# Kernel optimization log

Measured on AMD Instinct MI355X. Metric: run time of the kernel, lower is better.

The kernel has to match this reference:

```python
import jax, jax.numpy as jnp
import numpy as np

EPS = 1e-12  # torch F.normalize eps

def _l2norm(v, axis):
    n = jnp.sqrt(jnp.sum(v * v, axis=axis, keepdims=True))
    return v / jnp.maximum(n, EPS)

def setup_inputs() -> dict:
    key = jax.random.key(0)
    k1, k2, k3 = jax.random.split(key, 3)
    N, C, H, W, K = 64, 512, 32, 32, 64
    x = jax.random.normal(k1, (N, C, H, W), dtype=jnp.float32)
    conv_w = jax.random.normal(k2, (K, C), dtype=jnp.float32) * 0.05
    centroids = jax.random.uniform(k3, (K, C), dtype=jnp.float32)
    return {"x": x, "conv_w": conv_w, "centroids": centroids}

def reference(x, conv_w, centroids):
    N, C, H, W = x.shape
    K = centroids.shape[0]
    # descriptor-wise L2 normalization over channel dim
    x = _l2norm(x, axis=1)
    xf = x.reshape(N, C, H * W)                       # (N, C, S)
    # 1x1 conv (no bias) == per-pixel matmul, then softmax over clusters
    logits = jnp.einsum('kc,ncs->nks', conv_w, xf)    # (N, K, S)
    a = jax.nn.softmax(logits, axis=1)                # softmax over clusters
    # vlad[n,k,:] = sum_s a[n,k,s] * (x[n,:,s] - centroid[k])
    # = (a @ x^T) - centroid * sum_s a   -- two GEMM-like ops, no (N,K,C,S) tensor
    vlad = jnp.einsum('nks,ncs->nkc', a, xf) - a.sum(axis=-1)[..., None] * centroids[None, :, :]
    # intra-normalization per cluster, flatten, global L2 norm
    vlad = _l2norm(vlad, axis=2)
    vlad = vlad.reshape(N, K * C)
    vlad = _l2norm(vlad, axis=1)
    return vlad
```

## Files before the change

### kernel.cpp

```cpp
#include <hip/hip_runtime.h>
#include <hip/hip_bf16.h>
#include <math.h>

#define EPSF 1e-12f

typedef __attribute__((ext_vector_type(8))) short bf16x8;
typedef __attribute__((ext_vector_type(4))) float f32x4;
typedef __attribute__((ext_vector_type(4))) short short4v;
typedef __attribute__((ext_vector_type(4))) unsigned short ushort4v;

static __device__ __forceinline__ short f2bf(float f) {
  union { __hip_bfloat16 h; short s; } u;
  u.h = __float2bfloat16(f);
  return u.s;
}

__global__ __launch_bounds__(256) void k2_mfma(
    const float* __restrict__ x, const float* __restrict__ w,
    unsigned short* __restrict__ ap, float* __restrict__ suma) {
  __shared__ __align__(16) float xf[64][70];
  __shared__ __align__(16) short wb[64][72];
  __shared__ __align__(16) float red[4][64];
  __shared__ float invs[64];
  __shared__ float gmaxs[64];
  __shared__ float gsums[64];

  const int n = blockIdx.y;
  const int s0 = blockIdx.x << 6;
  const int t = threadIdx.x;
  const int lane = t & 63;
  const int wid = t >> 6;
  const int col = t & 15;
  const int quad = (t >> 4) & 3;
  const int cr = t >> 4;
  const int sg = t & 15;

  f32x4 acc[4] = {{0,0,0,0},{0,0,0,0},{0,0,0,0},{0,0,0,0}};
  float ssq0 = 0.f, ssq1 = 0.f, ssq2 = 0.f, ssq3 = 0.f;

  for (int c0 = 0; c0 < 512; c0 += 64) {
#pragma unroll
    for (int p = 0; p < 4; ++p) {
      int c = cr + (p << 4);
      float4 g = *(const float4*)&x[((size_t)((n << 9) + c0 + c) << 10) + s0 + (sg << 2)];
      float2 glo; glo.x = g.x; glo.y = g.y;
      float2 ghi; ghi.x = g.z; ghi.y = g.w;
      *(float2*)&xf[c][sg << 2] = glo;
      *(float2*)&xf[c][(sg << 2) + 2] = ghi;
      ssq0 = fmaf(g.x, g.x, ssq0); ssq1 = fmaf(g.y, g.y, ssq1);
      ssq2 = fmaf(g.z, g.z, ssq2); ssq3 = fmaf(g.w, g.w, ssq3);
      float4 gw = *(const float4*)&w[(c << 9) + c0 + (sg << 2)];
      short4v hw; hw.x = f2bf(gw.x); hw.y = f2bf(gw.y); hw.z = f2bf(gw.z); hw.w = f2bf(gw.w);
      *(short4v*)&wb[c][sg << 2] = hw;
    }
    __syncthreads();
#pragma unroll
    for (int cc = 0; cc < 64; cc += 32) {
      bf16x8 af = *(const bf16x8*)&wb[(wid << 4) + col][cc + (quad << 3)];
      int cb = cc + (quad << 3);
#pragma unroll
      for (int sgr = 0; sgr < 4; ++sgr) {
        int sc = (sgr << 4) + col;
        bf16x8 bfr;
#pragma unroll
        for (int j = 0; j < 8; ++j) bfr[j] = f2bf(xf[cb + j][sc]);
        acc[sgr] = __builtin_amdgcn_mfma_f32_16x16x32_bf16(af, bfr, acc[sgr], 0, 0, 0);
      }
    }
    __syncthreads();
  }

  ssq0 += __shfl_xor(ssq0, 16, 64); ssq0 += __shfl_xor(ssq0, 32, 64);
  ssq1 += __shfl_xor(ssq1, 16, 64); ssq1 += __shfl_xor(ssq1, 32, 64);
  ssq2 += __shfl_xor(ssq2, 16, 64); ssq2 += __shfl_xor(ssq2, 32, 64);
  ssq3 += __shfl_xor(ssq3, 16, 64); ssq3 += __shfl_xor(ssq3, 32, 64);
  if (lane < 16) {
    float4 v; v.x = ssq0; v.y = ssq1; v.z = ssq2; v.w = ssq3;
    *(float4*)&red[wid][sg << 2] = v;
  }
  __syncthreads();
  if (t < 64) {
    float tot = red[0][t] + red[1][t] + red[2][t] + red[3][t];
    invs[t] = 1.0f / fmaxf(sqrtf(tot), EPSF);
  }
  __syncthreads();

  float li[4];
#pragma unroll
  for (int sgr = 0; sgr < 4; ++sgr) li[sgr] = invs[(sgr << 4) + col];
  float le[4][4];
#pragma unroll
  for (int sgr = 0; sgr < 4; ++sgr)
#pragma unroll
    for (int r = 0; r < 4; ++r) le[sgr][r] = acc[sgr][r] * li[sgr];

  float mx[4];
#pragma unroll
  for (int sgr = 0; sgr < 4; ++sgr) {
    float m = fmaxf(fmaxf(le[sgr][0], le[sgr][1]), fmaxf(le[sgr][2], le[sgr][3]));
    m = fmaxf(m, __shfl_xor(m, 16, 64));
    m = fmaxf(m, __shfl_xor(m, 32, 64));
    mx[sgr] = m;
  }
  if (lane < 16) {
#pragma unroll
    for (int sgr = 0; sgr < 4; ++sgr) red[wid][(sgr << 4) + sg] = mx[sgr];
  }
  __syncthreads();
  if (t < 64)
    gmaxs[t] = fmaxf(fmaxf(red[0][t], red[1][t]), fmaxf(red[2][t], red[3][t]));
  __syncthreads();

  float ps[4];
#pragma unroll
  for (int sgr = 0; sgr < 4; ++sgr) {
    float gm = gmaxs[(sgr << 4) + col];
    float p = 0.f;
#pragma unroll
    for (int r = 0; r < 4; ++r) {
      float e = __expf(le[sgr][r] - gm);
      le[sgr][r] = e;
      p += e;
    }
    p += __shfl_xor(p, 16, 64);
    p += __shfl_xor(p, 32, 64);
    ps[sgr] = p;
  }
  if (lane < 16) {
#pragma unroll
    for (int sgr = 0; sgr < 4; ++sgr) red[wid][(sgr << 4) + sg] = ps[sgr];
  }
  __syncthreads();
  if (t < 64) gsums[t] = red[0][t] + red[1][t] + red[2][t] + red[3][t];
  __syncthreads();

  float sk[4] = {0.f, 0.f, 0.f, 0.f};
#pragma unroll
  for (int sgr = 0; sgr < 4; ++sgr) {
    float rinv = 1.0f / gsums[(sgr << 4) + col];
#pragma unroll
    for (int r = 0; r < 4; ++r) {
      float av = le[sgr][r] * rinv;
      sk[r] += av;
      float apv = av * li[sgr];
      int k = (wid << 4) + (quad << 2) + r;
      ap[((size_t)((n << 6) + k) << 10) + s0 + (sgr << 4) + col] =
          (unsigned short)f2bf(apv);
    }
  }
#pragma unroll
  for (int r = 0; r < 4; ++r) {
    sk[r] += __shfl_xor(sk[r], 1, 64);
    sk[r] += __shfl_xor(sk[r], 2, 64);
    sk[r] += __shfl_xor(sk[r], 4, 64);
    sk[r] += __shfl_xor(sk[r], 8, 64);
  }
  if (col == 0) {
#pragma unroll
    for (int r = 0; r < 4; ++r)
      atomicAdd(&suma[(n << 6) + (wid << 4) + (quad << 2) + r], sk[r]);
  }
}

#define K3_LOADT(gx, ga, S0)                                                   \
  do {                                                                         \
    _Pragma("unroll") for (int p = 0; p < 4; ++p) {                            \
      gx[p] = *(const float4*)(xbase + ((size_t)(p << 4) << 10) + (S0));       \
      ga[p] = *(const ushort4v*)(abase + ((size_t)(p << 4) << 10) + (S0));     \
    }                                                                          \
  } while (0)

#define K3_WRITET(gx, ga)                                                      \
  do {                                                                         \
    _Pragma("unroll") for (int p = 0; p < 4; ++p) {                            \
      int c = cr + (p << 4);                                                   \
      short4v hx;                                                              \
      hx.x = f2bf(gx[p].x); hx.y = f2bf(gx[p].y);                              \
      hx.z = f2bf(gx[p].z); hx.w = f2bf(gx[p].w);                              \
      *(short4v*)&xb[c][sg << 2] = hx;                                         \
      *(ushort4v*)&at[c][sg << 2] = ga[p];                                     \
    }                                                                          \
  } while (0)

#define K3_MFMAT()                                                             \
  do {                                                                         \
    _Pragma("unroll") for (int ss = 0; ss < 64; ss += 32) {                    \
      bf16x8 af = *(const bf16x8*)&xb[(wid << 4) + col][ss + (quad << 3)];     \
      _Pragma("unroll") for (int kt = 0; kt < 4; ++kt) {                       \
        bf16x8 bfr = *(const bf16x8*)&at[(kt << 4) + col][ss + (quad << 3)];   \
        acc[kt] = __builtin_amdgcn_mfma_f32_16x16x32_bf16(af, bfr, acc[kt], 0, 0, 0); \
      }                                                                        \
    }                                                                          \
  } while (0)

__global__ __launch_bounds__(256) void k3_mfma(
    const float* __restrict__ x, const unsigned short* __restrict__ ap,
    const float* __restrict__ cent, const float* __restrict__ suma,
    float* __restrict__ out, float* __restrict__ rnorm2) {
  __shared__ __align__(16) char sm[64 * 72 * 2 * 2];
  short (*xb)[72] = reinterpret_cast<short(*)[72]>(sm);
  short (*at)[72] = reinterpret_cast<short(*)[72]>(sm + 9216);
  float (*lt)[68] = reinterpret_cast<float(*)[68]>(sm);

  const int n = blockIdx.x;
  const int c0 = blockIdx.y << 6;
  const int t = threadIdx.x;
  const int lane = t & 63;
  const int wid = t >> 6;
  const int col = t & 15;
  const int quad = (t >> 4) & 3;
  const int cr = t >> 4;
  const int sg = t & 15;

  f32x4 acc[4] = {{0,0,0,0},{0,0,0,0},{0,0,0,0},{0,0,0,0}};

  const float* xbase = &x[((size_t)((n << 9) + c0 + cr) << 10) + (sg << 2)];
  const unsigned short* abase = &ap[((size_t)((n << 6) + cr) << 10) + (sg << 2)];

  float4 gxA[4]; ushort4v gaA[4];
  float4 gxB[4]; ushort4v gaB[4];

  K3_LOADT(gxA, gaA, 0);
#pragma unroll 1
  for (int it = 0; it < 8; ++it) {
    K3_WRITET(gxA, gaA);
    __syncthreads();
    K3_LOADT(gxB, gaB, (size_t)(((it << 1) + 1) << 6));
    K3_MFMAT();
    __syncthreads();
    K3_WRITET(gxB, gaB);
    __syncthreads();
    if (it < 7) {
      K3_LOADT(gxA, gaA, (size_t)(((it << 1) + 2) << 6));
    }
    K3_MFMAT();
    __syncthreads();
  }

  float sa[4];
#pragma unroll
  for (int kt = 0; kt < 4; ++kt) sa[kt] = suma[(n << 6) + (kt << 4) + col];
  const int crow = (wid << 4) + (quad << 2);
  float r2[4] = {0.f, 0.f, 0.f, 0.f};
#pragma unroll
  for (int kt = 0; kt < 4; ++kt) {
    int k = (kt << 4) + col;
#pragma unroll
    for (int r = 0; r < 4; ++r) {
      int c = crow + r;
      float ce = cent[(k << 9) + c0 + c];
      float val = acc[kt][r] - sa[kt] * ce;
      r2[kt] = fmaf(val, val, r2[kt]);
      lt[k][c] = val;
    }
  }
#pragma unroll
  for (int kt = 0; kt < 4; ++kt) {
    r2[kt] += __shfl_xor(r2[kt], 16, 64);
    r2[kt] += __shfl_xor(r2[kt], 32, 64);
  }
  if (lane < 16) {
#pragma unroll
    for (int kt = 0; kt < 4; ++kt)
      atomicAdd(&rnorm2[(n << 6) + (kt << 4) + sg], r2[kt]);
  }
  __syncthreads();
#pragma unroll
  for (int u = 0; u < 4; ++u) {
    int k = t >> 2;
    int c = ((t & 3) << 2) + (u << 4);
    float4 v = *(const float4*)&lt[k][c];
    *(float4*)&out[((size_t)((n << 6) + k) << 9) + c0 + c] = v;
  }
}

__global__ __launch_bounds__(256) void k5_scale(const float* __restrict__ vlad,
                                                const float* __restrict__ rnorm2,
                                                float* __restrict__ out) {
  __shared__ float gsh;
  const int b = blockIdx.x;
  const int t = threadIdx.x;
  const int n = b >> 5;
  if (t < 64) {
    float rn = sqrtf(rnorm2[(n << 6) + t]);
    float nr = rn / fmaxf(rn, EPSF);
    float g = nr * nr;
#pragma unroll
    for (int off = 32; off > 0; off >>= 1) g += __shfl_xor(g, off, 64);
    if (t == 0) gsh = g;
  }
  __syncthreads();
  const float ginv = 1.0f / fmaxf(sqrtf(gsh), EPSF);
  const int idx = (b << 8) + t;
  const int kg = idx >> 7;
  float rn = sqrtf(rnorm2[kg]);
  float f = (1.0f / fmaxf(rn, EPSF)) * ginv;
  float4 v = ((const float4*)vlad)[idx];
  float4 o;
  o.x = v.x * f; o.y = v.y * f; o.z = v.z * f; o.w = v.w * f;
  ((float4*)out)[idx] = o;
}

extern "C" void kernel_launch(void* const* d_in, const int* in_sizes, int n_in,
                              void* d_out, int out_size, void* d_ws, size_t ws_size,
                              hipStream_t stream) {
  (void)in_sizes; (void)n_in; (void)out_size; (void)ws_size;
  const float* x = (const float*)d_in[0];
  const float* w = (const float*)d_in[1];
  const float* cent = (const float*)d_in[2];
  float* out = (float*)d_out;

  float* ws = (float*)d_ws;
  float* suma = ws;
  float* rnorm2 = ws + 4096;
  unsigned short* ap = (unsigned short*)(ws + 12288);

  hipMemsetAsync(ws, 0, 8192 * sizeof(float), stream);
  k2_mfma<<<dim3(16, 64), 256, 0, stream>>>(x, w, ap, suma);
  k3_mfma<<<dim3(64, 8), 256, 0, stream>>>(x, ap, cent, suma, out, rnorm2);
  k5_scale<<<2048, 256, 0, stream>>>(out, rnorm2, out);
}
```

Before: 229.4 us.

## Halve k3 channel tile to 32, double grid, double-buffer LDS tiles

The second GEMM kernel now covers 32 channels per block instead of 64, which doubles the grid to 1024 blocks for better CU occupancy. Each wave now computes a 16x32 output sub-tile, and the 64-wide spatial tiles are double-buffered in shared memory, removing one barrier per stage. Launch bounds request four blocks per CU. The cost is that each assignment tile is re-read twice as often, and the per-block epilogue is smaller.

```diff
diff --git a/kernel.cpp b/kernel.cpp
--- a/kernel.cpp
+++ b/kernel.cpp
@@ -162,115 +162,118 @@
   }
 }
 
-#define K3_LOADT(gx, ga, S0)                                                   \
+#define K3_LOADT(GX0, GX1, GA0, GA1, TI)                                       \
   do {                                                                         \
-    _Pragma("unroll") for (int p = 0; p < 4; ++p) {                            \
-      gx[p] = *(const float4*)(xbase + ((size_t)(p << 4) << 10) + (S0));       \
-      ga[p] = *(const ushort4v*)(abase + ((size_t)(p << 4) << 10) + (S0));     \
-    }                                                                          \
+    const int so_ = (TI) << 6;                                                 \
+    GX0 = *(const float4*)(xbase + so_);                                       \
+    GX1 = *(const float4*)(xbase + so_ + 32);                                  \
+    GA0 = *(const bf16x8*)(abase + so_);                                       \
+    GA1 = *(const bf16x8*)(abase + so_ + 32);                                  \
   } while (0)
 
-#define K3_WRITET(gx, ga)                                                      \
+#define K3_WRITET(GX0, GX1, GA0, GA1, XB, AT)                                  \
   do {                                                                         \
-    _Pragma("unroll") for (int p = 0; p < 4; ++p) {                            \
-      int c = cr + (p << 4);                                                   \
-      short4v hx;                                                              \
-      hx.x = f2bf(gx[p].x); hx.y = f2bf(gx[p].y);                              \
-      hx.z = f2bf(gx[p].z); hx.w = f2bf(gx[p].w);                              \
-      *(short4v*)&xb[c][sg << 2] = hx;                                         \
-      *(ushort4v*)&at[c][sg << 2] = ga[p];                                     \
-    }                                                                          \
+    short4v h0, h1;                                                            \
+    h0.x = f2bf(GX0.x); h0.y = f2bf(GX0.y); h0.z = f2bf(GX0.z); h0.w = f2bf(GX0.w); \
+    h1.x = f2bf(GX1.x); h1.y = f2bf(GX1.y); h1.z = f2bf(GX1.z); h1.w = f2bf(GX1.w); \
+    *(short4v*)&XB[t >> 3][(t & 7) << 2] = h0;                                 \
+    *(short4v*)&XB[t >> 3][((t & 7) << 2) + 32] = h1;                          \
+    *(bf16x8*)&AT[t >> 2][(t & 3) << 3] = GA0;                                 \
+    *(bf16x8*)&AT[t >> 2][((t & 3) << 3) + 32] = GA1;                          \
   } while (0)
 
-#define K3_MFMAT()                                                             \
+#define K3_MFMAT(XB, AT)                                                       \
   do {                                                                         \
     _Pragma("unroll") for (int ss = 0; ss < 64; ss += 32) {                    \
-      bf16x8 af = *(const bf16x8*)&xb[(wid << 4) + col][ss + (quad << 3)];     \
-      _Pragma("unroll") for (int kt = 0; kt < 4; ++kt) {                       \
-        bf16x8 bfr = *(const bf16x8*)&at[(kt << 4) + col][ss + (quad << 3)];   \
+      bf16x8 af = *(const bf16x8*)&XB[cb + col][ss + (quad << 3)];             \
+      _Pragma("unroll") for (int kt = 0; kt < 2; ++kt) {                       \
+        bf16x8 bfr = *(const bf16x8*)&AT[kb + (kt << 4) + col][ss + (quad << 3)]; \
         acc[kt] = __builtin_amdgcn_mfma_f32_16x16x32_bf16(af, bfr, acc[kt], 0, 0, 0); \
       }                                                                        \
     }                                                                          \
   } while (0)
 
-__global__ __launch_bounds__(256) void k3_mfma(
+__global__ __launch_bounds__(256, 4) void k3_mfma(
     const float* __restrict__ x, const unsigned short* __restrict__ ap,
     const float* __restrict__ cent, const float* __restrict__ suma,
     float* __restrict__ out, float* __restrict__ rnorm2) {
-  __shared__ __align__(16) char sm[64 * 72 * 2 * 2];
-  short (*xb)[72] = reinterpret_cast<short(*)[72]>(sm);
-  short (*at)[72] = reinterpret_cast<short(*)[72]>(sm + 9216);
-  float (*lt)[68] = reinterpret_cast<float(*)[68]>(sm);
+  __shared__ __align__(16) char sm[27648];
+  short (*xb0)[72] = reinterpret_cast<short(*)[72]>(sm);
+  short (*at0)[72] = reinterpret_cast<short(*)[72]>(sm + 4608);
+  short (*xb1)[72] = reinterpret_cast<short(*)[72]>(sm + 13824);
+  short (*at1)[72] = reinterpret_cast<short(*)[72]>(sm + 18432);
+  float (*lt)[36] = reinterpret_cast<float(*)[36]>(sm);
 
   const int n = blockIdx.x;
-  const int c0 = blockIdx.y << 6;
+  const int c0 = blockIdx.y << 5;
   const int t = threadIdx.x;
   const int lane = t & 63;
   const int wid = t >> 6;
   const int col = t & 15;
   const int quad = (t >> 4) & 3;
-  const int cr = t >> 4;
   const int sg = t & 15;
-
-  f32x4 acc[4] = {{0,0,0,0},{0,0,0,0},{0,0,0,0},{0,0,0,0}};
-
-  const float* xbase = &x[((size_t)((n << 9) + c0 + cr) << 10) + (sg << 2)];
-  const unsigned short* abase = &ap[((size_t)((n << 6) + cr) << 10) + (sg << 2)];
-
-  float4 gxA[4]; ushort4v gaA[4];
-  float4 gxB[4]; ushort4v gaB[4];
-
-  K3_LOADT(gxA, gaA, 0);
+  const int cb = (wid & 1) << 4;
+  const int kb = (wid >> 1) << 5;
+
+  f32x4 acc[2] = {{0, 0, 0, 0}, {0, 0, 0, 0}};
+
+  const float* xbase = &x[((size_t)((n << 9) + c0 + (t >> 3)) << 10) + ((t & 7) << 2)];
+  const unsigned short* abase = &ap[((size_t)((n << 6) + (t >> 2)) << 10) + ((t & 3) << 3)];
+
+  float4 xA0, xA1, xB0, xB1;
+  bf16x8 aA0, aA1, aB0, aB1;
+
+  K3_LOADT(xA0, xA1, aA0, aA1, 0);
+  K3_WRITET(xA0, xA1, aA0, aA1, xb0, at0);
+  K3_LOADT(xB0, xB1, aB0, aB1, 1);
+  __syncthreads();
+
 #pragma unroll 1
-  for (int it = 0; it < 8; ++it) {
-    K3_WRITET(gxA, gaA);
+  for (int it = 0; it < 16; it += 2) {
+    const bool last = (it == 14);
+    K3_WRITET(xB0, xB1, aB0, aB1, xb1, at1);
+    if (!last) K3_LOADT(xA0, xA1, aA0, aA1, it + 2);
+    K3_MFMAT(xb0, at0);
     __syncthreads();
-    K3_LOADT(gxB, gaB, (size_t)(((it << 1) + 1) << 6));
-    K3_MFMAT();
+    if (!last) {
+      K3_WRITET(xA0, xA1, aA0, aA1, xb0, at0);
+      K3_LOADT(xB0, xB1, aB0, aB1, it + 3);
+    }
+    K3_MFMAT(xb1, at1);
     __syncthreads();
-    K3_WRITET(gxB, gaB);
-    __syncthreads();
-    if (it < 7) {
-      K3_LOADT(gxA, gaA, (size_t)(((it << 1) + 2) << 6));
-    }
-    K3_MFMAT();
-    __syncthreads();
-  }
-
-  float sa[4];
-#pragma unroll
-  for (int kt = 0; kt < 4; ++kt) sa[kt] = suma[(n << 6) + (kt << 4) + col];
-  const int crow = (wid << 4) + (quad << 2);
-  float r2[4] = {0.f, 0.f, 0.f, 0.f};
-#pragma unroll
-  for (int kt = 0; kt < 4; ++kt) {
-    int k = (kt << 4) + col;
-#pragma unroll
-    for (int r = 0; r < 4; ++r) {
-      int c = crow + r;
-      float ce = cent[(k << 9) + c0 + c];
-      float val = acc[kt][r] - sa[kt] * ce;
-      r2[kt] = fmaf(val, val, r2[kt]);
-      lt[k][c] = val;
-    }
-  }
-#pragma unroll
-  for (int kt = 0; kt < 4; ++kt) {
-    r2[kt] += __shfl_xor(r2[kt], 16, 64);
-    r2[kt] += __shfl_xor(r2[kt], 32, 64);
-  }
+  }
+
+  const float sa0 = suma[(n << 6) + kb + col];
+  const float sa1 = suma[(n << 6) + kb + 16 + col];
+  const int crow = cb + (quad << 2);
+  const int k0 = kb + col;
+  const int k1 = kb + 16 + col;
+  float r2_0 = 0.f, r2_1 = 0.f;
+#pragma unroll
+  for (int r = 0; r < 4; ++r) {
+    int c = crow + r;
+    float ce0 = cent[(k0 << 9) + c0 + c];
+    float v0 = acc[0][r] - sa0 * ce0;
+    r2_0 = fmaf(v0, v0, r2_0);
+    lt[k0][c] = v0;
+    float ce1 = cent[(k1 << 9) + c0 + c];
+    float v1 = acc[1][r] - sa1 * ce1;
+    r2_1 = fmaf(v1, v1, r2_1);
+    lt[k1][c] = v1;
+  }
+  r2_0 += __shfl_xor(r2_0, 16, 64); r2_0 += __shfl_xor(r2_0, 32, 64);
+  r2_1 += __shfl_xor(r2_1, 16, 64); r2_1 += __shfl_xor(r2_1, 32, 64);
   if (lane < 16) {
-#pragma unroll
-    for (int kt = 0; kt < 4; ++kt)
-      atomicAdd(&rnorm2[(n << 6) + (kt << 4) + sg], r2[kt]);
-  }
-  __syncthreads();
-#pragma unroll
-  for (int u = 0; u < 4; ++u) {
-    int k = t >> 2;
+    atomicAdd(&rnorm2[(n << 6) + kb + sg], r2_0);
+    atomicAdd(&rnorm2[(n << 6) + kb + 16 + sg], r2_1);
+  }
+  __syncthreads();
+#pragma unroll
+  for (int u = 0; u < 2; ++u) {
+    int kk = t >> 2;
     int c = ((t & 3) << 2) + (u << 4);
-    float4 v = *(const float4*)&lt[k][c];
-    *(float4*)&out[((size_t)((n << 6) + k) << 9) + c0 + c] = v;
+    float4 v = *(const float4*)&lt[kk][c];
+    *(float4*)&out[((size_t)((n << 6) + kk) << 9) + c0 + c] = v;
   }
 }
 
@@ -317,6 +320,6 @@
 
   hipMemsetAsync(ws, 0, 8192 * sizeof(float), stream);
   k2_mfma<<<dim3(16, 64), 256, 0, stream>>>(x, w, ap, suma);
-  k3_mfma<<<dim3(64, 8), 256, 0, stream>>>(x, ap, cent, suma, out, rnorm2);
+  k3_mfma<<<dim3(64, 16), 256, 0, stream>>>(x, ap, cent, suma, out, rnorm2);
   k5_scale<<<2048, 256, 0, stream>>>(out, rnorm2, out);
 }
```

After: 228.3 us. No clear change (-0.5%).
